# Kernel optimization log

Hardware: AMD Instinct MI355X
Metric: run time of the kernel (lower is better)

Reference implementation:

```python
import jax, jax.numpy as jnp
import numpy as np

N_NODES = 50000

def _sage(x, src, dst, Wl, bl, Wr):
    # PyG SAGEConv(aggr='mean'): out = lin_l(mean_{j in N(i)} x_j) + lin_r(x_i)
    msg = x[src]                                                    # [E, F] gather
    agg = jax.ops.segment_sum(msg, dst, num_segments=N_NODES)      # [N, F]
    cnt = jax.ops.segment_sum(jnp.ones((src.shape[0],), x.dtype), dst, num_segments=N_NODES)
    agg = agg / jnp.maximum(cnt, 1.0)[:, None]                     # mean aggregate
    return agg @ Wl + bl + x @ Wr                                   # lin_l has bias, lin_r does not


def setup_inputs() -> dict:
    key = jax.random.key(0)
    ks = jax.random.split(key, 14)
    d_in, d_h, d_out, n_edges = 128, 64, 4, 800000
    s = lambda k, shp, fan: jax.random.normal(k, shp, jnp.float32) * (1.0 / np.sqrt(fan))
    return {
        'x': jax.random.normal(ks[0], (N_NODES, d_in), jnp.float32),
        'edge_index': jax.random.randint(ks[1], (2, n_edges), 0, N_NODES, jnp.int64),
        'Wl1': s(ks[2], (d_in, d_h), d_in), 'bl1': jnp.zeros((d_h,), jnp.float32),
        'Wr1': s(ks[3], (d_in, d_h), d_in),
        'Wl2': s(ks[4], (d_h, d_h), d_h), 'bl2': jnp.zeros((d_h,), jnp.float32),
        'Wr2': s(ks[5], (d_h, d_h), d_h),
        'Wl3': s(ks[6], (d_h, d_h), d_h), 'bl3': jnp.zeros((d_h,), jnp.float32),
        'Wr3': s(ks[7], (d_h, d_h), d_h),
        'Wp': s(ks[8], (2 * d_h, d_out), 2 * d_h), 'bp': jnp.zeros((d_out,), jnp.float32),
    }


def reference(x, edge_index, Wl1, bl1, Wr1, Wl2, bl2, Wr2, Wl3, bl3, Wr3, Wp, bp):
    src, dst = edge_index[0], edge_index[1]
    # dropout is identity in eval mode
    h = jax.nn.elu(_sage(x, src, dst, Wl1, bl1, Wr1))
    h = jax.nn.elu(_sage(h, src, dst, Wl2, bl2, Wr2))
    h = jax.nn.elu(_sage(h, src, dst, Wl3, bl3, Wr3))
    edge_feat = jnp.concatenate([h[src], h[dst]], axis=1)  # [E, 2*hidden]
    return edge_feat @ Wp + bp                              # [E, output_dim]
```

## Files before the change

### kernel.cpp

```cpp
#include <hip/hip_runtime.h>
#include <hip/hip_bf16.h>

#define N_NODES 50000
#define N_EDGES 800000
#define D_IN 128
#define D_H 64
#define SCAN_BLOCKS 196
#define HIST_BLOCKS 3125
#define LIN1_BLOCKS 782
#define GL_BLOCKS 3125

#define F1L 0
#define F1R 8192
#define F2L 16384
#define F2R 20480
#define F3L 24576
#define F3R 28672
#define FRAG_TOTAL 32768

typedef short bf16x8 __attribute__((ext_vector_type(8)));
typedef float f32x4 __attribute__((ext_vector_type(4)));

__device__ __forceinline__ ushort f2bf(float f) {
    __hip_bfloat16 b = __float2bfloat16(f);
    return *reinterpret_cast<ushort*>(&b);
}
__device__ __forceinline__ float bf16_lo(unsigned int u) { return __uint_as_float(u << 16); }
__device__ __forceinline__ float bf16_hi(unsigned int u) { return __uint_as_float(u & 0xffff0000u); }

__device__ __forceinline__ void build_frag_one(const float* __restrict__ W, int local,
                                               ushort* __restrict__ frag, int fid) {
    int lane = local & 63;
    int ktnt = local >> 6;
    int kt = ktnt >> 2, nt = ktnt & 3;
    int quad = lane >> 4, col = lane & 15;
    ushort t0 = f2bf(W[(kt * 32 + quad * 8 + 0) * D_H + nt * 16 + col]);
    ushort t1 = f2bf(W[(kt * 32 + quad * 8 + 1) * D_H + nt * 16 + col]);
    ushort t2 = f2bf(W[(kt * 32 + quad * 8 + 2) * D_H + nt * 16 + col]);
    ushort t3 = f2bf(W[(kt * 32 + quad * 8 + 3) * D_H + nt * 16 + col]);
    ushort t4 = f2bf(W[(kt * 32 + quad * 8 + 4) * D_H + nt * 16 + col]);
    ushort t5 = f2bf(W[(kt * 32 + quad * 8 + 5) * D_H + nt * 16 + col]);
    ushort t6 = f2bf(W[(kt * 32 + quad * 8 + 6) * D_H + nt * 16 + col]);
    ushort t7 = f2bf(W[(kt * 32 + quad * 8 + 7) * D_H + nt * 16 + col]);
    uint4 v;
    v.x = (unsigned int)t0 | ((unsigned int)t1 << 16);
    v.y = (unsigned int)t2 | ((unsigned int)t3 << 16);
    v.z = (unsigned int)t4 | ((unsigned int)t5 << 16);
    v.w = (unsigned int)t6 | ((unsigned int)t7 << 16);
    *reinterpret_cast<uint4*>(frag + (size_t)fid * 8) = v;
}

__global__ void hist_frags_kernel(const int* __restrict__ dstv, int* __restrict__ cnt,
                                  ushort* __restrict__ rank,
                                  const float* __restrict__ Wl1, const float* __restrict__ Wr1,
                                  const float* __restrict__ Wl2, const float* __restrict__ Wr2,
                                  const float* __restrict__ Wl3, const float* __restrict__ Wr3,
                                  ushort* __restrict__ frag) {
    if (blockIdx.x < HIST_BLOCKS) {
        int e = blockIdx.x * 256 + threadIdx.x;
        if (e < N_EDGES) {
            int r = atomicAdd(&cnt[dstv[e]], 1);
            rank[e] = (ushort)r;
        }
    } else {
        int fid = (blockIdx.x - HIST_BLOCKS) * 256 + threadIdx.x;
        const float* W; int base;
        if (fid < 1024)      { W = Wl1; base = 0; }
        else if (fid < 2048) { W = Wr1; base = 1024; }
        else if (fid < 2560) { W = Wl2; base = 2048; }
        else if (fid < 3072) { W = Wr2; base = 2560; }
        else if (fid < 3584) { W = Wl3; base = 3072; }
        else                 { W = Wr3; base = 3584; }
        build_frag_one(W, fid - base, frag, fid);
    }
}

__global__ void scan_partial(const int* __restrict__ cnt, int* __restrict__ blockSums) {
    __shared__ int s[256];
    int i = blockIdx.x * 256 + threadIdx.x;
    s[threadIdx.x] = (i < N_NODES) ? cnt[i] : 0;
    __syncthreads();
    for (int off = 128; off > 0; off >>= 1) {
        if (threadIdx.x < off) s[threadIdx.x] += s[threadIdx.x + off];
        __syncthreads();
    }
    if (threadIdx.x == 0) blockSums[blockIdx.x] = s[0];
}

__global__ void scan_final(const int* __restrict__ cnt, const int* __restrict__ blockSums,
                           int* __restrict__ row_ptr) {
    __shared__ int s[256];
    __shared__ int bs[256];
    int t = threadIdx.x;
    bs[t] = (t < SCAN_BLOCKS) ? blockSums[t] : 0;
    int i = blockIdx.x * 256 + t;
    s[t] = (i < N_NODES) ? cnt[i] : 0;
    __syncthreads();
    for (int off = 1; off < 256; off <<= 1) {
        int tmp1 = (t >= off) ? s[t - off] : 0;
        int tmp2 = (t >= off) ? bs[t - off] : 0;
        __syncthreads();
        s[t] += tmp1;
        bs[t] += tmp2;
        __syncthreads();
    }
    int blockExcl = (blockIdx.x > 0) ? bs[blockIdx.x - 1] : 0;
    int excl = blockExcl + ((t > 0) ? s[t - 1] : 0);
    if (i < N_NODES) row_ptr[i] = excl;
    if (i == 0) row_ptr[N_NODES] = N_EDGES;
}

__device__ __forceinline__ void lin1_body(int gwave, int lane, const float* __restrict__ hin,
                                          const ushort* __restrict__ fragWl,
                                          const ushort* __restrict__ fragWr,
                                          ushort* __restrict__ Y, ushort* __restrict__ Zb) {
    constexpr int KT = D_IN / 32;
    int m0 = gwave * 16;
    if (m0 >= N_NODES) return;
    int col = lane & 15;
    int quad = lane >> 4;

    bf16x8 blf[KT], brf[KT][4];
    bf16x8 blf2[KT][4];
#pragma unroll
    for (int kt = 0; kt < KT; ++kt)
#pragma unroll
        for (int nt = 0; nt < 4; ++nt) {
            size_t off = (size_t)((kt * 4 + nt) * 64 + lane) * 8;
            blf2[kt][nt] = __builtin_bit_cast(bf16x8, *reinterpret_cast<const uint4*>(fragWl + off));
            brf[kt][nt] = __builtin_bit_cast(bf16x8, *reinterpret_cast<const uint4*>(fragWr + off));
        }

    f32x4 accl0 = {0.f,0.f,0.f,0.f}, accl1 = accl0, accl2 = accl0, accl3 = accl0;
    f32x4 accr0 = accl0, accr1 = accl0, accr2 = accl0, accr3 = accl0;
    const float* arow = hin + (size_t)(m0 + col) * D_IN + quad * 8;
#pragma unroll
    for (int kt = 0; kt < KT; ++kt) {
        float4 a_lo = *reinterpret_cast<const float4*>(arow + kt * 32);
        float4 a_hi = *reinterpret_cast<const float4*>(arow + kt * 32 + 4);
        bf16x8 a;
        a[0] = (short)f2bf(a_lo.x); a[1] = (short)f2bf(a_lo.y);
        a[2] = (short)f2bf(a_lo.z); a[3] = (short)f2bf(a_lo.w);
        a[4] = (short)f2bf(a_hi.x); a[5] = (short)f2bf(a_hi.y);
        a[6] = (short)f2bf(a_hi.z); a[7] = (short)f2bf(a_hi.w);
        accl0 = __builtin_amdgcn_mfma_f32_16x16x32_bf16(a, blf2[kt][0], accl0, 0, 0, 0);
        accl1 = __builtin_amdgcn_mfma_f32_16x16x32_bf16(a, blf2[kt][1], accl1, 0, 0, 0);
        accl2 = __builtin_amdgcn_mfma_f32_16x16x32_bf16(a, blf2[kt][2], accl2, 0, 0, 0);
        accl3 = __builtin_amdgcn_mfma_f32_16x16x32_bf16(a, blf2[kt][3], accl3, 0, 0, 0);
        accr0 = __builtin_amdgcn_mfma_f32_16x16x32_bf16(a, brf[kt][0], accr0, 0, 0, 0);
        accr1 = __builtin_amdgcn_mfma_f32_16x16x32_bf16(a, brf[kt][1], accr1, 0, 0, 0);
        accr2 = __builtin_amdgcn_mfma_f32_16x16x32_bf16(a, brf[kt][2], accr2, 0, 0, 0);
        accr3 = __builtin_amdgcn_mfma_f32_16x16x32_bf16(a, brf[kt][3], accr3, 0, 0, 0);
    }
#pragma unroll
    for (int reg = 0; reg < 4; ++reg) {
        size_t r = (size_t)(m0 + quad * 4 + reg) * D_H;
        ushort* yp = Y + r;
        yp[0 * 16 + col] = f2bf(accl0[reg]);
        yp[1 * 16 + col] = f2bf(accl1[reg]);
        yp[2 * 16 + col] = f2bf(accl2[reg]);
        yp[3 * 16 + col] = f2bf(accl3[reg]);
        ushort* zp = Zb + r;
        zp[0 * 16 + col] = f2bf(accr0[reg]);
        zp[1 * 16 + col] = f2bf(accr1[reg]);
        zp[2 * 16 + col] = f2bf(accr2[reg]);
        zp[3 * 16 + col] = f2bf(accr3[reg]);
    }
}

__global__ void lin1_fill_kernel(const float* __restrict__ x, const ushort* __restrict__ wfrag,
                                 const int* __restrict__ srcv, const int* __restrict__ dstv,
                                 const ushort* __restrict__ rank, const int* __restrict__ row_ptr,
                                 ushort* __restrict__ csr_src,
                                 ushort* __restrict__ Y, ushort* __restrict__ Zb) {
    if (blockIdx.x < LIN1_BLOCKS) {
        int gwave = (blockIdx.x * 256 + threadIdx.x) >> 6;
        lin1_body(gwave, threadIdx.x & 63, x, wfrag + F1L, wfrag + F1R, Y, Zb);
    } else {
        int e = (blockIdx.x - LIN1_BLOCKS) * 256 + threadIdx.x;
        if (e < N_EDGES) {
            int d = dstv[e];
            int pos = row_ptr[d] + (int)rank[e];
            csr_src[pos] = (ushort)srcv[e];
        }
    }
}

template <bool FUSE_PROJ>
__global__ void gather_lin_kernel(const ushort* __restrict__ Y, const ushort* __restrict__ Zb,
                                  const float* __restrict__ bl,
                                  const int* __restrict__ row_ptr, const ushort* __restrict__ csr_src,
                                  const ushort* __restrict__ fragWl, const ushort* __restrict__ fragWr,
                                  ushort* __restrict__ Ynext, ushort* __restrict__ Zbnext,
                                  const float* __restrict__ Wp,
                                  float* __restrict__ ps, float* __restrict__ pd) {
    __shared__ ushort Hs[16][72];
    int w = threadIdx.x >> 6;
    int lane = threadIdx.x & 63;
    int wv = (blockIdx.x << 2) + w;
    int n0 = wv << 2;
    int g = lane >> 4;
    int l = lane & 15;

    int rp[5];
#pragma unroll
    for (int i = 0; i < 5; ++i) rp[i] = row_ptr[n0 + i];
    int deg[4];
#pragma unroll
    for (int n = 0; n < 4; ++n) deg[n] = rp[n + 1] - rp[n];
    int maxdeg = deg[0];
#pragma unroll
    for (int n = 1; n < 4; ++n) maxdeg = deg[n] > maxdeg ? deg[n] : maxdeg;

    float acc[4][4] = {{0.f}};
    const uint2* __restrict__ Y2 = reinterpret_cast<const uint2*>(Y);

    for (int base = 0; base < maxdeg; base += 64) {
        int idxv[4];
#pragma unroll
        for (int n = 0; n < 4; ++n) idxv[n] = (int)csr_src[rp[n] + base + lane];
        int wend[4];
#pragma unroll
        for (int n = 0; n < 4; ++n) { wend[n] = deg[n] - base; if (wend[n] > 64) wend[n] = 64; }
        int kmax = wend[0];
#pragma unroll
        for (int n = 1; n < 4; ++n) kmax = wend[n] > kmax ? wend[n] : kmax;
        for (int k = 0; k < kmax; k += 16) {
            uint2 rr[4][4];
#pragma unroll
            for (int n = 0; n < 4; ++n)
#pragma unroll
                for (int j = 0; j < 4; ++j) {
                    int s = __shfl(idxv[n], k + 4 * j + g);
                    rr[n][j] = Y2[s * 16 + l];
                }
#pragma unroll
            for (int n = 0; n < 4; ++n)
#pragma unroll
                for (int j = 0; j < 4; ++j) {
                    if (k + 4 * j + g < wend[n]) {
                        acc[n][0] += bf16_lo(rr[n][j].x); acc[n][1] += bf16_hi(rr[n][j].x);
                        acc[n][2] += bf16_lo(rr[n][j].y); acc[n][3] += bf16_hi(rr[n][j].y);
                    }
                }
        }
    }

#pragma unroll
    for (int n = 0; n < 4; ++n)
#pragma unroll
        for (int f = 0; f < 4; ++f) {
            acc[n][f] += __shfl_xor(acc[n][f], 16);
            acc[n][f] += __shfl_xor(acc[n][f], 32);
        }

    int node = n0 + g;
    float dgf = (g == 0) ? (float)deg[0] : (g == 1) ? (float)deg[1]
              : (g == 2) ? (float)deg[2] : (float)deg[3];
    float c0 = (g == 0) ? acc[0][0] : (g == 1) ? acc[1][0] : (g == 2) ? acc[2][0] : acc[3][0];
    float c1 = (g == 0) ? acc[0][1] : (g == 1) ? acc[1][1] : (g == 2) ? acc[2][1] : acc[3][1];
    float c2 = (g == 0) ? acc[0][2] : (g == 1) ? acc[1][2] : (g == 2) ? acc[2][2] : acc[3][2];
    float c3 = (g == 0) ? acc[0][3] : (g == 1) ? acc[1][3] : (g == 2) ? acc[2][3] : acc[3][3];
    float inv = 1.0f / fmaxf(dgf, 1.0f);
    float4 bv = reinterpret_cast<const float4*>(bl)[l];
    uint2 zr = reinterpret_cast<const uint2*>(Zb)[node * 16 + l];
    float v0 = c0 * inv + bv.x + bf16_lo(zr.x);
    float v1 = c1 * inv + bv.y + bf16_hi(zr.x);
    float v2 = c2 * inv + bv.z + bf16_lo(zr.y);
    float v3 = c3 * inv + bv.w + bf16_hi(zr.y);
    float o0 = v0 > 0.f ? v0 : expm1f(v0);
    float o1 = v1 > 0.f ? v1 : expm1f(v1);
    float o2 = v2 > 0.f ? v2 : expm1f(v2);
    float o3 = v3 > 0.f ? v3 : expm1f(v3);

    if constexpr (FUSE_PROJ) {
        float p0 = 0.f, p1 = 0.f, p2 = 0.f, p3 = 0.f;
        float q0 = 0.f, q1 = 0.f, q2 = 0.f, q3 = 0.f;
        float ov[4] = {o0, o1, o2, o3};
#pragma unroll
        for (int j = 0; j < 4; ++j) {
            int k = 4 * l + j;
            float4 wt = reinterpret_cast<const float4*>(Wp)[k];
            float4 wb = reinterpret_cast<const float4*>(Wp)[D_H + k];
            p0 += ov[j] * wt.x; p1 += ov[j] * wt.y; p2 += ov[j] * wt.z; p3 += ov[j] * wt.w;
            q0 += ov[j] * wb.x; q1 += ov[j] * wb.y; q2 += ov[j] * wb.z; q3 += ov[j] * wb.w;
        }
#pragma unroll
        for (int off = 1; off < 16; off <<= 1) {
            p0 += __shfl_xor(p0, off); p1 += __shfl_xor(p1, off);
            p2 += __shfl_xor(p2, off); p3 += __shfl_xor(p3, off);
            q0 += __shfl_xor(q0, off); q1 += __shfl_xor(q1, off);
            q2 += __shfl_xor(q2, off); q3 += __shfl_xor(q3, off);
        }
        if (l == 0) {
            float4 pv; pv.x = p0; pv.y = p1; pv.z = p2; pv.w = p3;
            float4 qv; qv.x = q0; qv.y = q1; qv.z = q2; qv.w = q3;
            reinterpret_cast<float4*>(ps)[node] = pv;
            reinterpret_cast<float4*>(pd)[node] = qv;
        }
    } else {
        ushort4 ob;
        ob.x = f2bf(o0); ob.y = f2bf(o1); ob.z = f2bf(o2); ob.w = f2bf(o3);
        int localrow = w * 4 + g;
        *reinterpret_cast<ushort4*>(&Hs[localrow][4 * l]) = ob;
        __syncthreads();

        int col = lane & 15;
        int quad = lane >> 4;
        bf16x8 blf0 = __builtin_bit_cast(bf16x8,
            *reinterpret_cast<const uint4*>(fragWl + (size_t)((0 * 4 + w) * 64 + lane) * 8));
        bf16x8 blf1 = __builtin_bit_cast(bf16x8,
            *reinterpret_cast<const uint4*>(fragWl + (size_t)((1 * 4 + w) * 64 + lane) * 8));
        bf16x8 brf0 = __builtin_bit_cast(bf16x8,
            *reinterpret_cast<const uint4*>(fragWr + (size_t)((0 * 4 + w) * 64 + lane) * 8));
        bf16x8 brf1 = __builtin_bit_cast(bf16x8,
            *reinterpret_cast<const uint4*>(fragWr + (size_t)((1 * 4 + w) * 64 + lane) * 8));
        bf16x8 a0 = __builtin_bit_cast(bf16x8,
            *reinterpret_cast<const uint4*>(&Hs[col][quad * 8]));
        bf16x8 a1 = __builtin_bit_cast(bf16x8,
            *reinterpret_cast<const uint4*>(&Hs[col][32 + quad * 8]));
        f32x4 accl = {0.f,0.f,0.f,0.f};
        f32x4 accr = {0.f,0.f,0.f,0.f};
        accl = __builtin_amdgcn_mfma_f32_16x16x32_bf16(a0, blf0, accl, 0, 0, 0);
        accl = __builtin_amdgcn_mfma_f32_16x16x32_bf16(a1, blf1, accl, 0, 0, 0);
        accr = __builtin_amdgcn_mfma_f32_16x16x32_bf16(a0, brf0, accr, 0, 0, 0);
        accr = __builtin_amdgcn_mfma_f32_16x16x32_bf16(a1, brf1, accr, 0, 0, 0);

        int n0base = blockIdx.x * 16;
#pragma unroll
        for (int reg = 0; reg < 4; ++reg) {
            size_t r = (size_t)(n0base + quad * 4 + reg) * D_H + w * 16 + col;
            Ynext[r]  = f2bf(accl[reg]);
            Zbnext[r] = f2bf(accr[reg]);
        }
    }
}

__global__ void edge_final_kernel(const int* __restrict__ srcv, const int* __restrict__ dstv,
                                  const float* __restrict__ ps, const float* __restrict__ pd,
                                  const float* __restrict__ bp, float* __restrict__ out) {
    int e = blockIdx.x * 256 + threadIdx.x;
    if (e >= N_EDGES) return;
    float4 a = reinterpret_cast<const float4*>(ps)[srcv[e]];
    float4 b = reinterpret_cast<const float4*>(pd)[dstv[e]];
    float4 o;
    o.x = a.x + b.x + bp[0];
    o.y = a.y + b.y + bp[1];
    o.z = a.z + b.z + bp[2];
    o.w = a.w + b.w + bp[3];
    reinterpret_cast<float4*>(out)[e] = o;
}

extern "C" void kernel_launch(void* const* d_in, const int* in_sizes, int n_in,
                              void* d_out, int out_size, void* d_ws, size_t ws_size,
                              hipStream_t stream) {
    const float* x   = (const float*)d_in[0];
    const int*   ei  = (const int*)d_in[1];
    const float* Wl1 = (const float*)d_in[2];
    const float* bl1 = (const float*)d_in[3];
    const float* Wr1 = (const float*)d_in[4];
    const float* Wl2 = (const float*)d_in[5];
    const float* bl2 = (const float*)d_in[6];
    const float* Wr2 = (const float*)d_in[7];
    const float* Wl3 = (const float*)d_in[8];
    const float* bl3 = (const float*)d_in[9];
    const float* Wr3 = (const float*)d_in[10];
    const float* Wp  = (const float*)d_in[11];
    const float* bp  = (const float*)d_in[12];
    float* out = (float*)d_out;

    const int* srcv = ei;
    const int* dstv = ei + N_EDGES;

    int*   cnt       = (int*)d_ws;
    int*   blockSums = cnt + 50000;
    int*   row_ptr   = blockSums + 256;
    ushort* rank     = (ushort*)(row_ptr + 50001);
    ushort* csr_src  = rank + 800000;
    ushort* wfrag = (ushort*)(((uintptr_t)(csr_src + 800000 + 4096) + 127) & ~(uintptr_t)127);
    ushort* Y1  = (ushort*)(((uintptr_t)(wfrag + FRAG_TOTAL) + 127) & ~(uintptr_t)127);
    ushort* Zb1 = Y1 + (size_t)N_NODES * D_H;
    ushort* Y2  = Zb1 + (size_t)N_NODES * D_H;
    ushort* Zb2 = Y2 + (size_t)N_NODES * D_H;
    float* ps = (float*)(((uintptr_t)(Zb2 + (size_t)N_NODES * D_H) + 15) & ~(uintptr_t)15);
    float* pd = ps + (size_t)N_NODES * 4;

    hipMemsetAsync(cnt, 0, N_NODES * sizeof(int), stream);
    hist_frags_kernel<<<HIST_BLOCKS + 16, 256, 0, stream>>>(dstv, cnt, rank, Wl1, Wr1, Wl2, Wr2,
                                                            Wl3, Wr3, wfrag);
    scan_partial<<<SCAN_BLOCKS, 256, 0, stream>>>(cnt, blockSums);
    scan_final<<<SCAN_BLOCKS, 256, 0, stream>>>(cnt, blockSums, row_ptr);

    lin1_fill_kernel<<<LIN1_BLOCKS + HIST_BLOCKS, 256, 0, stream>>>(x, wfrag, srcv, dstv,
                                                                    rank, row_ptr, csr_src,
                                                                    Y1, Zb1);

    gather_lin_kernel<false><<<GL_BLOCKS, 256, 0, stream>>>(Y1, Zb1, bl1, row_ptr, csr_src,
                                                            wfrag + F2L, wfrag + F2R, Y2, Zb2,
                                                            nullptr, nullptr, nullptr);

    gather_lin_kernel<false><<<GL_BLOCKS, 256, 0, stream>>>(Y2, Zb2, bl2, row_ptr, csr_src,
                                                            wfrag + F3L, wfrag + F3R, Y1, Zb1,
                                                            nullptr, nullptr, nullptr);

    gather_lin_kernel<true><<<GL_BLOCKS, 256, 0, stream>>>(Y1, Zb1, bl3, row_ptr, csr_src,
                                                           nullptr, nullptr, nullptr, nullptr,
                                                           Wp, ps, pd);

    edge_final_kernel<<<(N_EDGES + 255) / 256, 256, 0, stream>>>(srcv, dstv, ps, pd, bp, out);
}
```

Baseline: 232.8 us.

## Overlap layer-1 linear with histogram, single-block scan, separate CSR fill

Reorganises the preprocessing pipeline. Layer-1 linear now runs in the same launch as the edge histogram, with per-block LDS weight fragments built in place. The two-kernel scan becomes one 1024-thread single-block scan, and the CSR fill moves to its own kernel. Also skips shuffles and loads for empty neighbour groups in the gather and folds the output bias into ps. This cuts launch count and lets the dense GEMM overlap the atomic histogram, at the cost of each lin1 block rebuilding the weight fragments and a serial single-block scan.

After: 332.9 us. 43.0% more time.

```diff
diff --git a/kernel.cpp b/kernel.cpp
--- a/kernel.cpp
+++ b/kernel.cpp
@@ -5,18 +5,16 @@
 #define N_EDGES 800000
 #define D_IN 128
 #define D_H 64
-#define SCAN_BLOCKS 196
 #define HIST_BLOCKS 3125
 #define LIN1_BLOCKS 782
+#define FRAG_BLOCKS 8
 #define GL_BLOCKS 3125
 
-#define F1L 0
-#define F1R 8192
-#define F2L 16384
-#define F2R 20480
-#define F3L 24576
-#define F3R 28672
-#define FRAG_TOTAL 32768
+#define F2L 0
+#define F2R 4096
+#define F3L 8192
+#define F3R 12288
+#define FRAG_TOTAL 16384
 
 typedef short bf16x8 __attribute__((ext_vector_type(8)));
 typedef float f32x4 __attribute__((ext_vector_type(4)));
@@ -50,69 +48,8 @@
     *reinterpret_cast<uint4*>(frag + (size_t)fid * 8) = v;
 }
 
-__global__ void hist_frags_kernel(const int* __restrict__ dstv, int* __restrict__ cnt,
-                                  ushort* __restrict__ rank,
-                                  const float* __restrict__ Wl1, const float* __restrict__ Wr1,
-                                  const float* __restrict__ Wl2, const float* __restrict__ Wr2,
-                                  const float* __restrict__ Wl3, const float* __restrict__ Wr3,
-                                  ushort* __restrict__ frag) {
-    if (blockIdx.x < HIST_BLOCKS) {
-        int e = blockIdx.x * 256 + threadIdx.x;
-        if (e < N_EDGES) {
-            int r = atomicAdd(&cnt[dstv[e]], 1);
-            rank[e] = (ushort)r;
-        }
-    } else {
-        int fid = (blockIdx.x - HIST_BLOCKS) * 256 + threadIdx.x;
-        const float* W; int base;
-        if (fid < 1024)      { W = Wl1; base = 0; }
-        else if (fid < 2048) { W = Wr1; base = 1024; }
-        else if (fid < 2560) { W = Wl2; base = 2048; }
-        else if (fid < 3072) { W = Wr2; base = 2560; }
-        else if (fid < 3584) { W = Wl3; base = 3072; }
-        else                 { W = Wr3; base = 3584; }
-        build_frag_one(W, fid - base, frag, fid);
-    }
-}
-
-__global__ void scan_partial(const int* __restrict__ cnt, int* __restrict__ blockSums) {
-    __shared__ int s[256];
-    int i = blockIdx.x * 256 + threadIdx.x;
-    s[threadIdx.x] = (i < N_NODES) ? cnt[i] : 0;
-    __syncthreads();
-    for (int off = 128; off > 0; off >>= 1) {
-        if (threadIdx.x < off) s[threadIdx.x] += s[threadIdx.x + off];
-        __syncthreads();
-    }
-    if (threadIdx.x == 0) blockSums[blockIdx.x] = s[0];
-}
-
-__global__ void scan_final(const int* __restrict__ cnt, const int* __restrict__ blockSums,
-                           int* __restrict__ row_ptr) {
-    __shared__ int s[256];
-    __shared__ int bs[256];
-    int t = threadIdx.x;
-    bs[t] = (t < SCAN_BLOCKS) ? blockSums[t] : 0;
-    int i = blockIdx.x * 256 + t;
-    s[t] = (i < N_NODES) ? cnt[i] : 0;
-    __syncthreads();
-    for (int off = 1; off < 256; off <<= 1) {
-        int tmp1 = (t >= off) ? s[t - off] : 0;
-        int tmp2 = (t >= off) ? bs[t - off] : 0;
-        __syncthreads();
-        s[t] += tmp1;
-        bs[t] += tmp2;
-        __syncthreads();
-    }
-    int blockExcl = (blockIdx.x > 0) ? bs[blockIdx.x - 1] : 0;
-    int excl = blockExcl + ((t > 0) ? s[t - 1] : 0);
-    if (i < N_NODES) row_ptr[i] = excl;
-    if (i == 0) row_ptr[N_NODES] = N_EDGES;
-}
-
 __device__ __forceinline__ void lin1_body(int gwave, int lane, const float* __restrict__ hin,
-                                          const ushort* __restrict__ fragWl,
-                                          const ushort* __restrict__ fragWr,
+                                          const ushort* fl, const ushort* fr,
                                           ushort* __restrict__ Y, ushort* __restrict__ Zb) {
     constexpr int KT = D_IN / 32;
     int m0 = gwave * 16;
@@ -120,19 +57,12 @@
     int col = lane & 15;
     int quad = lane >> 4;
 
-    bf16x8 blf[KT], brf[KT][4];
-    bf16x8 blf2[KT][4];
-#pragma unroll
-    for (int kt = 0; kt < KT; ++kt)
-#pragma unroll
-        for (int nt = 0; nt < 4; ++nt) {
-            size_t off = (size_t)((kt * 4 + nt) * 64 + lane) * 8;
-            blf2[kt][nt] = __builtin_bit_cast(bf16x8, *reinterpret_cast<const uint4*>(fragWl + off));
-            brf[kt][nt] = __builtin_bit_cast(bf16x8, *reinterpret_cast<const uint4*>(fragWr + off));
-        }
-
-    f32x4 accl0 = {0.f,0.f,0.f,0.f}, accl1 = accl0, accl2 = accl0, accl3 = accl0;
-    f32x4 accr0 = accl0, accr1 = accl0, accr2 = accl0, accr3 = accl0;
+    f32x4 accl[4], accr[4];
+#pragma unroll
+    for (int nt = 0; nt < 4; ++nt) {
+        accl[nt] = (f32x4){0.f, 0.f, 0.f, 0.f};
+        accr[nt] = (f32x4){0.f, 0.f, 0.f, 0.f};
+    }
     const float* arow = hin + (size_t)(m0 + col) * D_IN + quad * 8;
 #pragma unroll
     for (int kt = 0; kt < KT; ++kt) {
@@ -143,46 +73,102 @@
         a[2] = (short)f2bf(a_lo.z); a[3] = (short)f2bf(a_lo.w);
         a[4] = (short)f2bf(a_hi.x); a[5] = (short)f2bf(a_hi.y);
         a[6] = (short)f2bf(a_hi.z); a[7] = (short)f2bf(a_hi.w);
-        accl0 = __builtin_amdgcn_mfma_f32_16x16x32_bf16(a, blf2[kt][0], accl0, 0, 0, 0);
-        accl1 = __builtin_amdgcn_mfma_f32_16x16x32_bf16(a, blf2[kt][1], accl1, 0, 0, 0);
-        accl2 = __builtin_amdgcn_mfma_f32_16x16x32_bf16(a, blf2[kt][2], accl2, 0, 0, 0);
-        accl3 = __builtin_amdgcn_mfma_f32_16x16x32_bf16(a, blf2[kt][3], accl3, 0, 0, 0);
-        accr0 = __builtin_amdgcn_mfma_f32_16x16x32_bf16(a, brf[kt][0], accr0, 0, 0, 0);
-        accr1 = __builtin_amdgcn_mfma_f32_16x16x32_bf16(a, brf[kt][1], accr1, 0, 0, 0);
-        accr2 = __builtin_amdgcn_mfma_f32_16x16x32_bf16(a, brf[kt][2], accr2, 0, 0, 0);
-        accr3 = __builtin_amdgcn_mfma_f32_16x16x32_bf16(a, brf[kt][3], accr3, 0, 0, 0);
+#pragma unroll
+        for (int nt = 0; nt < 4; ++nt) {
+            size_t off = (size_t)((kt * 4 + nt) * 64 + lane) * 8;
+            bf16x8 bl = __builtin_bit_cast(bf16x8, *reinterpret_cast<const uint4*>(fl + off));
+            bf16x8 br = __builtin_bit_cast(bf16x8, *reinterpret_cast<const uint4*>(fr + off));
+            accl[nt] = __builtin_amdgcn_mfma_f32_16x16x32_bf16(a, bl, accl[nt], 0, 0, 0);
+            accr[nt] = __builtin_amdgcn_mfma_f32_16x16x32_bf16(a, br, accr[nt], 0, 0, 0);
+        }
     }
 #pragma unroll
     for (int reg = 0; reg < 4; ++reg) {
         size_t r = (size_t)(m0 + quad * 4 + reg) * D_H;
         ushort* yp = Y + r;
-        yp[0 * 16 + col] = f2bf(accl0[reg]);
-        yp[1 * 16 + col] = f2bf(accl1[reg]);
-        yp[2 * 16 + col] = f2bf(accl2[reg]);
-        yp[3 * 16 + col] = f2bf(accl3[reg]);
         ushort* zp = Zb + r;
-        zp[0 * 16 + col] = f2bf(accr0[reg]);
-        zp[1 * 16 + col] = f2bf(accr1[reg]);
-        zp[2 * 16 + col] = f2bf(accr2[reg]);
-        zp[3 * 16 + col] = f2bf(accr3[reg]);
-    }
-}
-
-__global__ void lin1_fill_kernel(const float* __restrict__ x, const ushort* __restrict__ wfrag,
-                                 const int* __restrict__ srcv, const int* __restrict__ dstv,
-                                 const ushort* __restrict__ rank, const int* __restrict__ row_ptr,
-                                 ushort* __restrict__ csr_src,
-                                 ushort* __restrict__ Y, ushort* __restrict__ Zb) {
+#pragma unroll
+        for (int nt = 0; nt < 4; ++nt) {
+            yp[nt * 16 + col] = f2bf(accl[nt][reg]);
+            zp[nt * 16 + col] = f2bf(accr[nt][reg]);
+        }
+    }
+}
+
+__global__ void k1_kernel(const float* __restrict__ x,
+                          const float* __restrict__ Wl1, const float* __restrict__ Wr1,
+                          const float* __restrict__ Wl2, const float* __restrict__ Wr2,
+                          const float* __restrict__ Wl3, const float* __restrict__ Wr3,
+                          const int* __restrict__ dstv, int* __restrict__ cnt,
+                          ushort* __restrict__ rank, ushort* __restrict__ wfrag,
+                          ushort* __restrict__ Y, ushort* __restrict__ Zb) {
+    __shared__ ushort fl[8192];
+    __shared__ ushort fr[8192];
     if (blockIdx.x < LIN1_BLOCKS) {
+#pragma unroll
+        for (int i = 0; i < 4; ++i) {
+            int local = i * 256 + threadIdx.x;
+            build_frag_one(Wl1, local, fl, local);
+            build_frag_one(Wr1, local, fr, local);
+        }
+        __syncthreads();
         int gwave = (blockIdx.x * 256 + threadIdx.x) >> 6;
-        lin1_body(gwave, threadIdx.x & 63, x, wfrag + F1L, wfrag + F1R, Y, Zb);
+        lin1_body(gwave, threadIdx.x & 63, x, fl, fr, Y, Zb);
+    } else if (blockIdx.x < LIN1_BLOCKS + FRAG_BLOCKS) {
+        int fid = (blockIdx.x - LIN1_BLOCKS) * 256 + threadIdx.x;
+        const float* W; int base;
+        if (fid < 512)       { W = Wl2; base = 0; }
+        else if (fid < 1024) { W = Wr2; base = 512; }
+        else if (fid < 1536) { W = Wl3; base = 1024; }
+        else                 { W = Wr3; base = 1536; }
+        build_frag_one(W, fid - base, wfrag, fid);
     } else {
-        int e = (blockIdx.x - LIN1_BLOCKS) * 256 + threadIdx.x;
+        int e = (blockIdx.x - LIN1_BLOCKS - FRAG_BLOCKS) * 256 + threadIdx.x;
         if (e < N_EDGES) {
-            int d = dstv[e];
-            int pos = row_ptr[d] + (int)rank[e];
-            csr_src[pos] = (ushort)srcv[e];
-        }
+            int r = atomicAdd(&cnt[dstv[e]], 1);
+            rank[e] = (ushort)r;
+        }
+    }
+}
+
+__global__ __launch_bounds__(1024) void scan_all(const int* __restrict__ cnt,
+                                                 int* __restrict__ row_ptr) {
+    __shared__ int s[1024];
+    constexpr int PER = 49;
+    int t = threadIdx.x;
+    int base = t * PER;
+    int sum = 0;
+    for (int i = 0; i < PER; ++i) {
+        int idx = base + i;
+        sum += (idx < N_NODES) ? cnt[idx] : 0;
+    }
+    s[t] = sum;
+    __syncthreads();
+    for (int off = 1; off < 1024; off <<= 1) {
+        int tmp = (t >= off) ? s[t - off] : 0;
+        __syncthreads();
+        s[t] += tmp;
+        __syncthreads();
+    }
+    int run = (t > 0) ? s[t - 1] : 0;
+    for (int i = 0; i < PER; ++i) {
+        int idx = base + i;
+        if (idx < N_NODES) {
+            row_ptr[idx] = run;
+            run += cnt[idx];
+        }
+    }
+    if (t == 0) row_ptr[N_NODES] = N_EDGES;
+}
+
+__global__ void fill_kernel(const int* __restrict__ srcv, const int* __restrict__ dstv,
+                            const ushort* __restrict__ rank, const int* __restrict__ row_ptr,
+                            ushort* __restrict__ csr_src) {
+    int e = blockIdx.x * 256 + threadIdx.x;
+    if (e < N_EDGES) {
+        int d = dstv[e];
+        int pos = row_ptr[d] + (int)rank[e];
+        csr_src[pos] = (ushort)srcv[e];
     }
 }
 
@@ -192,7 +178,7 @@
                                   const int* __restrict__ row_ptr, const ushort* __restrict__ csr_src,
                                   const ushort* __restrict__ fragWl, const ushort* __restrict__ fragWr,
                                   ushort* __restrict__ Ynext, ushort* __restrict__ Zbnext,
-                                  const float* __restrict__ Wp,
+                                  const float* __restrict__ Wp, const float* __restrict__ bp,
                                   float* __restrict__ ps, float* __restrict__ pd) {
     __shared__ ushort Hs[16][72];
     int w = threadIdx.x >> 6;
@@ -228,21 +214,28 @@
         for (int k = 0; k < kmax; k += 16) {
             uint2 rr[4][4];
 #pragma unroll
-            for (int n = 0; n < 4; ++n)
-#pragma unroll
-                for (int j = 0; j < 4; ++j) {
-                    int s = __shfl(idxv[n], k + 4 * j + g);
-                    rr[n][j] = Y2[s * 16 + l];
-                }
-#pragma unroll
-            for (int n = 0; n < 4; ++n)
-#pragma unroll
-                for (int j = 0; j < 4; ++j) {
-                    if (k + 4 * j + g < wend[n]) {
-                        acc[n][0] += bf16_lo(rr[n][j].x); acc[n][1] += bf16_hi(rr[n][j].x);
-                        acc[n][2] += bf16_lo(rr[n][j].y); acc[n][3] += bf16_hi(rr[n][j].y);
+            for (int n = 0; n < 4; ++n) {
+                if (k < wend[n]) {
+#pragma unroll
+                    for (int j = 0; j < 4; ++j) {
+                        int s = __shfl(idxv[n], k + 4 * j + g);
+                        if (k + 4 * j + g < wend[n])
+                            rr[n][j] = Y2[s * 16 + l];
                     }
                 }
+            }
+#pragma unroll
+            for (int n = 0; n < 4; ++n) {
+                if (k < wend[n]) {
+#pragma unroll
+                    for (int j = 0; j < 4; ++j) {
+                        if (k + 4 * j + g < wend[n]) {
+                            acc[n][0] += bf16_lo(rr[n][j].x); acc[n][1] += bf16_hi(rr[n][j].x);
+                            acc[n][2] += bf16_lo(rr[n][j].y); acc[n][3] += bf16_hi(rr[n][j].y);
+                        }
+                    }
+                }
+            }
         }
     }
 
@@ -293,7 +286,8 @@
             q2 += __shfl_xor(q2, off); q3 += __shfl_xor(q3, off);
         }
         if (l == 0) {
-            float4 pv; pv.x = p0; pv.y = p1; pv.z = p2; pv.w = p3;
+            float4 bpv = *reinterpret_cast<const float4*>(bp);
+            float4 pv; pv.x = p0 + bpv.x; pv.y = p1 + bpv.y; pv.z = p2 + bpv.z; pv.w = p3 + bpv.w;
             float4 qv; qv.x = q0; qv.y = q1; qv.z = q2; qv.w = q3;
             reinterpret_cast<float4*>(ps)[node] = pv;
             reinterpret_cast<float4*>(pd)[node] = qv;
@@ -338,16 +332,16 @@
 
 __global__ void edge_final_kernel(const int* __restrict__ srcv, const int* __restrict__ dstv,
                                   const float* __restrict__ ps, const float* __restrict__ pd,
-                                  const float* __restrict__ bp, float* __restrict__ out) {
+                                  float* __restrict__ out) {
     int e = blockIdx.x * 256 + threadIdx.x;
     if (e >= N_EDGES) return;
     float4 a = reinterpret_cast<const float4*>(ps)[srcv[e]];
     float4 b = reinterpret_cast<const float4*>(pd)[dstv[e]];
     float4 o;
-    o.x = a.x + b.x + bp[0];
-    o.y = a.y + b.y + bp[1];
-    o.z = a.z + b.z + bp[2];
-    o.w = a.w + b.w + bp[3];
+    o.x = a.x + b.x;
+    o.y = a.y + b.y;
+    o.z = a.z + b.z;
+    o.w = a.w + b.w;
     reinterpret_cast<float4*>(out)[e] = o;
 }
 
@@ -386,26 +380,24 @@
     float* pd = ps + (size_t)N_NODES * 4;
 
     hipMemsetAsync(cnt, 0, N_NODES * sizeof(int), stream);
-    hist_frags_kernel<<<HIST_BLOCKS + 16, 256, 0, stream>>>(dstv, cnt, rank, Wl1, Wr1, Wl2, Wr2,
-                                                            Wl3, Wr3, wfrag);
-    scan_partial<<<SCAN_BLOCKS, 256, 0, stream>>>(cnt, blockSums);
-    scan_final<<<SCAN_BLOCKS, 256, 0, stream>>>(cnt, blockSums, row_ptr);
-
-    lin1_fill_kernel<<<LIN1_BLOCKS + HIST_BLOCKS, 256, 0, stream>>>(x, wfrag, srcv, dstv,
-                                                                    rank, row_ptr, csr_src,
-                                                                    Y1, Zb1);
+    k1_kernel<<<LIN1_BLOCKS + FRAG_BLOCKS + HIST_BLOCKS, 256, 0, stream>>>(
+        x, Wl1, Wr1, Wl2, Wr2, Wl3, Wr3, dstv, cnt, rank, wfrag, Y1, Zb1);
+
+    scan_all<<<1, 1024, 0, stream>>>(cnt, row_ptr);
+
+    fill_kernel<<<HIST_BLOCKS, 256, 0, stream>>>(srcv, dstv, rank, row_ptr, csr_src);
 
     gather_lin_kernel<false><<<GL_BLOCKS, 256, 0, stream>>>(Y1, Zb1, bl1, row_ptr, csr_src,
                                                             wfrag + F2L, wfrag + F2R, Y2, Zb2,
-                                                            nullptr, nullptr, nullptr);
+                                                            nullptr, nullptr, nullptr, nullptr);
 
     gather_lin_kernel<false><<<GL_BLOCKS, 256, 0, stream>>>(Y2, Zb2, bl2, row_ptr, csr_src,
                                                             wfrag + F3L, wfrag + F3R, Y1, Zb1,
-                                                            nullptr, nullptr, nullptr);
+                                                            nullptr, nullptr, nullptr, nullptr);
 
     gather_lin_kernel<true><<<GL_BLOCKS, 256, 0, stream>>>(Y1, Zb1, bl3, row_ptr, csr_src,
                                                            nullptr, nullptr, nullptr, nullptr,
-                                                           Wp, ps, pd);
-
-    edge_final_kernel<<<(N_EDGES + 255) / 256, 256, 0, stream>>>(srcv, dstv, ps, pd, bp, out);
-}
+                                                           Wp, bp, ps, pd);
+
+    edge_final_kernel<<<(N_EDGES + 255) / 256, 256, 0, stream>>>(srcv, dstv, ps, pd, out);
+}
```
